# Kernel tuning notes

Measured on AMD Instinct MI355X. Metric: run time of the kernel, lower is better.

The kernel has to match this reference:

```python
import jax, jax.numpy as jnp
import numpy as np

N, E, H, G, L = 50000, 640000, 128, 8, 3

def setup_inputs() -> dict:
    key = jax.random.key(0)
    ks = jax.random.split(key, 10)
    s = 1.0 / np.sqrt(H)
    return {
        "x": jax.random.normal(ks[0], (N, H), jnp.float32),
        "query": jax.random.normal(ks[1], (G, H), jnp.float32),
        "Wl": jax.random.normal(ks[2], (L, H, H), jnp.float32) * s,
        "bl": jax.random.normal(ks[3], (L, H), jnp.float32) * s,
        "Wr": jax.random.normal(ks[4], (L, H, H), jnp.float32) * s,
        "Wlin": jax.random.normal(ks[5], (H, H), jnp.float32) * s,
        "blin": jax.random.normal(ks[6], (H,), jnp.float32) * s,
        "edge_index": jax.random.randint(ks[7], (2, E), 0, N, jnp.int64),
        "batch_vec": jnp.sort(jax.random.randint(ks[8], (N,), 0, G, jnp.int64)),
    }

def reference(x, query, Wl, bl, Wr, Wlin, blin, edge_index, batch_vec):
    src, dst = edge_index[0], edge_index[1]
    n = x.shape[0]
    for i in range(L):
        # SAGEConv(aggr='max'): gather neighbor feats, scatter-max to dst
        m = jax.ops.segment_max(x[src], dst, num_segments=n)  # [N,H]
        m = jnp.where(jnp.isfinite(m), m, 0.0)  # isolated nodes -> 0 (PyG)
        x = jax.nn.relu(m @ Wl[i].T + bl[i] + x @ Wr[i].T)
    x = x @ Wlin.T + blin  # encoder final linear
    # cosine scoring per graph, vectorized via batch_vec
    xn = x / jnp.linalg.norm(x, axis=1, keepdims=True).clip(1e-12)
    qn = query / jnp.linalg.norm(query, axis=1, keepdims=True).clip(1e-12)
    scores = jnp.sum(xn * qn[batch_vec], axis=1)  # [N]
    return scores
```

## Files before the change

kernel.cpp:

```cpp
#include <hip/hip_runtime.h>
#include <math.h>

#define H 128

typedef _Float16 half8 __attribute__((ext_vector_type(8)));
typedef float f32x16 __attribute__((ext_vector_type(16)));

__device__ __forceinline__ half8 h8max(half8 a, half8 b) {
#if defined(__has_builtin) && __has_builtin(__builtin_elementwise_max)
    return __builtin_elementwise_max(a, b);
#else
    half8 r;
#pragma unroll
    for (int j = 0; j < 8; ++j) r[j] = a[j] > b[j] ? a[j] : b[j];
    return r;
#endif
}


__global__ __launch_bounds__(256) void hist_deg(const int* __restrict__ ei, int E,
                                                int* __restrict__ deg) {
    int e = blockIdx.x * 256 + threadIdx.x;
    if (e < E) atomicAdd(&deg[ei[E + e]], 1);
}

__global__ __launch_bounds__(256) void scan_atomic(const int* __restrict__ deg,
                                                   int* __restrict__ offsets,
                                                   int* __restrict__ gcur, int N) {
    __shared__ int buf[256];
    __shared__ int sbase;
    int tid = threadIdx.x;
    int i = blockIdx.x * 256 + tid;
    int v = (i < N) ? deg[i] : 0;
    int incl = v;
    buf[tid] = v;
    __syncthreads();
#pragma unroll
    for (int off = 1; off < 256; off <<= 1) {
        int t = (tid >= off) ? buf[tid - off] : 0;
        __syncthreads();
        incl += t;
        buf[tid] = incl;
        __syncthreads();
    }
    if (tid == 255) sbase = atomicAdd(gcur, incl);
    __syncthreads();
    if (i < N) offsets[i] = sbase + incl - v;
}

__global__ __launch_bounds__(256) void fill_adj(const int* __restrict__ ei, int E,
                                                const int* __restrict__ offsets,
                                                int* __restrict__ cursor,
                                                int* __restrict__ adj) {
    int e = blockIdx.x * 256 + threadIdx.x;
    if (e < E) {
        int s = ei[e];
        int d = ei[E + e];
        int pos = atomicAdd(&cursor[d], 1);
        adj[offsets[d] + pos] = s;
    }
}


__global__ __launch_bounds__(256) void prep_all(
    const float* __restrict__ x, const float* __restrict__ query,
    const float* __restrict__ Wl, const float* __restrict__ Wr,
    const float* __restrict__ Wlin, _Float16* __restrict__ xh,
    _Float16* __restrict__ wimg, float* __restrict__ qn, int n8, int SB, int WB) {
    int b = blockIdx.x;
    int tid = threadIdx.x;
    if (b < SB) {
        int i = b * 256 + tid;
        if (i < n8) {
            const float4* x4 = (const float4*)x;
            float4 u = x4[(size_t)i * 2], v = x4[(size_t)i * 2 + 1];
            float f[8] = {u.x, u.y, u.z, u.w, v.x, v.y, v.z, v.w};
            half8 h;
#pragma unroll
            for (int j = 0; j < 8; ++j) h[j] = (_Float16)f[j];
            *(half8*)(xh + (size_t)i * 8) = h;
        }
    } else if (b < SB + WB) {
        int gidx = (b - SB) * 256 + tid;
        if (gidx < 7 * 2048) {
            int mat = gidx / 2048;
            int rem = gidx - mat * 2048;
            int n = rem >> 4;
            int g = rem & 15;
            const float* src = (mat == 6) ? Wlin
                             : ((mat & 1) ? Wr + (mat >> 1) * H * H
                                          : Wl + (mat >> 1) * H * H);
            const float* p = src + n * H + g * 8;
            half8 h, l;
#pragma unroll
            for (int j = 0; j < 8; ++j) {
                float v = p[j];
                _Float16 hh = (_Float16)v;
                h[j] = hh;
                l[j] = (_Float16)(v - (float)hh);
            }
            int kc4 = g >> 2, gpc = g & 3;
            int posB = (gpc + (n & 3) + ((n >> 2) & 3)) & 3;
            size_t base = (size_t)mat * 32768 + (size_t)kc4 * 8192 + n * 32 + posB * 8;
            *(half8*)(wimg + base) = h;
            *(half8*)(wimg + base + 4096) = l;
        }
    } else {
        int g = b - SB - WB;
        __shared__ float part[4];
        float v = (tid < 128) ? query[g * H + tid] : 0.f;
        float ss = v * v;
#pragma unroll
        for (int off = 32; off > 0; off >>= 1) ss += __shfl_xor(ss, off, 64);
        if ((tid & 63) == 0) part[tid >> 6] = ss;
        __syncthreads();
        float tot = part[0] + part[1];
        if (tid < 128) qn[g * H + tid] = v / fmaxf(sqrtf(tot), 1e-12f);
    }
}


__global__ __launch_bounds__(256) void layer_fused2(
    const half8* __restrict__ Xh, const int* __restrict__ deg,
    const int* __restrict__ offsets, const int* __restrict__ adj,
    const _Float16* __restrict__ Bimg, const float* __restrict__ bias,
    _Float16* __restrict__ Yh, int N) {
    __shared__ __align__(16) _Float16 sU[8192];
    __shared__ __align__(16) _Float16 sB[8192];

    int tid = threadIdx.x;
    int w = tid >> 6;
    int lane = tid & 63;
    int l31 = lane & 31;
    int lhi = lane >> 5;
    int ws = w >> 1;
    int wc = w & 1;
    int n0 = blockIdx.x * 64;

    {
        int lf = tid & 15;
        int grp = tid >> 4;
        const _Float16 ni = (_Float16)(-INFINITY);
        const half8 ninf = {ni, ni, ni, ni, ni, ni, ni, ni};
        const half8 hz = {(_Float16)0.f, (_Float16)0.f, (_Float16)0.f, (_Float16)0.f,
                          (_Float16)0.f, (_Float16)0.f, (_Float16)0.f, (_Float16)0.f};
#pragma unroll
        for (int pp = 0; pp < 2; ++pp) {
            int rowA = grp * 4 + pp * 2;
            int rowB = rowA + 1;
            int nA = n0 + rowA, nB = n0 + rowB;
            int eA = 0, dA = 0, eB = 0, dB = 0;
            if (nA < N) { eA = offsets[nA]; dA = deg[nA]; }
            if (nB < N) { eB = offsets[nB]; dB = deg[nB]; }
            half8 a0 = ninf, a1 = ninf, b0 = ninf, b1 = ninf;
            int itm = dA > dB ? dA : dB;
            for (int base = 0; base < itm; base += 4) {
                bool doA = base < dA, doB = base < dB;
                half8 vA[4], vB[4];
                if (doA) {
#pragma unroll
                    for (int u = 0; u < 4; ++u) {
                        int ee = base + u;
                        int idx = adj[eA + (ee < dA ? ee : dA - 1)];
                        vA[u] = Xh[(size_t)idx * 16 + lf];
                    }
                }
                if (doB) {
#pragma unroll
                    for (int u = 0; u < 4; ++u) {
                        int ee = base + u;
                        int idx = adj[eB + (ee < dB ? ee : dB - 1)];
                        vB[u] = Xh[(size_t)idx * 16 + lf];
                    }
                }
                if (doA) {
                    a0 = h8max(a0, h8max(vA[0], vA[2]));
                    a1 = h8max(a1, h8max(vA[1], vA[3]));
                }
                if (doB) {
                    b0 = h8max(b0, h8max(vB[0], vB[2]));
                    b1 = h8max(b1, h8max(vB[1], vB[3]));
                }
            }
            half8 bestA = (dA > 0) ? h8max(a0, a1) : hz;
            half8 bestB = (dB > 0) ? h8max(b0, b1) : hz;
            *(half8*)&sU[rowA * 128 + (lf ^ (rowA & 15)) * 8] = bestA;
            *(half8*)&sU[rowB * 128 + (lf ^ (rowB & 15)) * 8] = bestB;
        }
    }
    __syncthreads();

    f32x16 acc[2];
#pragma unroll
    for (int nt = 0; nt < 2; ++nt) {
        float bv = bias[wc * 64 + nt * 32 + l31];
#pragma unroll
        for (int r = 0; r < 16; ++r) acc[nt][r] = bv;
    }

    int rl = ws * 32 + l31;

    for (int kc4 = 0; kc4 < 4; ++kc4) {
        if (kc4) __syncthreads();
        {
            const half8* bsrc = (const half8*)(Bimg + (size_t)kc4 * 8192);
            half8* bdst = (half8*)sB;
#pragma unroll
            for (int i = 0; i < 4; ++i) bdst[tid + i * 256] = bsrc[tid + i * 256];
        }
        __syncthreads();
#pragma unroll
        for (int ks = 0; ks < 2; ++ks) {
            int g16 = kc4 * 4 + ks * 2 + lhi;
            int posA = g16 ^ (rl & 15);
            half8 ah = *(const half8*)&sU[rl * 128 + posA * 8];
#pragma unroll
            for (int nt = 0; nt < 2; ++nt) {
                int n = wc * 64 + nt * 32 + l31;
                int gpc = ks * 2 + lhi;
                int posB = (gpc + (n & 3) + ((n >> 2) & 3)) & 3;
                half8 bh = *(const half8*)&sB[n * 32 + posB * 8];
                half8 bl = *(const half8*)&sB[4096 + n * 32 + posB * 8];
                acc[nt] = __builtin_amdgcn_mfma_f32_32x32x16_f16(ah, bh, acc[nt], 0, 0, 0);
                acc[nt] = __builtin_amdgcn_mfma_f32_32x32x16_f16(ah, bl, acc[nt], 0, 0, 0);
            }
        }
    }

    for (int kc4 = 0; kc4 < 4; ++kc4) {
        __syncthreads();
        {
            const half8* bsrc = (const half8*)(Bimg + 32768 + (size_t)kc4 * 8192);
            half8* bdst = (half8*)sB;
#pragma unroll
            for (int i = 0; i < 4; ++i) bdst[tid + i * 256] = bsrc[tid + i * 256];
        }
        if ((kc4 & 1) == 0) {
            int kc64 = kc4 >> 1;
#pragma unroll
            for (int i = 0; i < 2; ++i) {
                int idx = tid + i * 256;
                int row = idx >> 3;
                int gp8 = idx & 7;
                int n = n0 + row;
                half8 h = {(_Float16)0.f, (_Float16)0.f, (_Float16)0.f, (_Float16)0.f,
                           (_Float16)0.f, (_Float16)0.f, (_Float16)0.f, (_Float16)0.f};
                if (n < N) h = Xh[(size_t)n * 16 + kc64 * 8 + gp8];
                int pos8 = (gp8 + (row & 7) + ((row >> 3) & 7)) & 7;
                *(half8*)&sU[row * 72 + pos8 * 8] = h;
            }
        }
        __syncthreads();
#pragma unroll
        for (int ks = 0; ks < 2; ++ks) {
            int gp8 = (kc4 & 1) * 4 + ks * 2 + lhi;
            int posA8 = (gp8 + (rl & 7) + ((rl >> 3) & 7)) & 7;
            half8 ah = *(const half8*)&sU[rl * 72 + posA8 * 8];
#pragma unroll
            for (int nt = 0; nt < 2; ++nt) {
                int n = wc * 64 + nt * 32 + l31;
                int gpc = ks * 2 + lhi;
                int posB = (gpc + (n & 3) + ((n >> 2) & 3)) & 3;
                half8 bh = *(const half8*)&sB[n * 32 + posB * 8];
                half8 bl = *(const half8*)&sB[4096 + n * 32 + posB * 8];
                acc[nt] = __builtin_amdgcn_mfma_f32_32x32x16_f16(ah, bh, acc[nt], 0, 0, 0);
                acc[nt] = __builtin_amdgcn_mfma_f32_32x32x16_f16(ah, bl, acc[nt], 0, 0, 0);
            }
        }
    }

#pragma unroll
    for (int r = 0; r < 16; ++r) {
        int row = n0 + ws * 32 + (r & 3) + 8 * (r >> 2) + 4 * lhi;
        if (row < N) {
#pragma unroll
            for (int nt = 0; nt < 2; ++nt) {
                int col = wc * 64 + nt * 32 + l31;
                Yh[(size_t)row * H + col] = (_Float16)fmaxf(acc[nt][r], 0.f);
            }
        }
    }
}


__global__ __launch_bounds__(256) void final_mfma6(
    const half8* __restrict__ Xh, const _Float16* __restrict__ Bimg,
    const float* __restrict__ blin, const float* __restrict__ qn,
    const int* __restrict__ bv, float* __restrict__ out, int N) {
    __shared__ __align__(16) _Float16 sA[9216];
    __shared__ __align__(16) _Float16 sB[8192];

    int tid = threadIdx.x;
    int w = tid >> 6;
    int lane = tid & 63;
    int l31 = lane & 31;
    int lhi = lane >> 5;
    int n0 = blockIdx.x * 128;

    int arow = n0 + w * 32 + l31;
    arow = arow < N ? arow : N - 1;
    int gl = bv[arow];

    f32x16 acc[4];
#pragma unroll
    for (int nt = 0; nt < 4; ++nt) {
        float b = blin[nt * 32 + l31];
#pragma unroll
        for (int r = 0; r < 16; ++r) acc[nt][r] = b;
    }

    int rl = w * 32 + l31;

    for (int kc4 = 0; kc4 < 4; ++kc4) {
        if (kc4) __syncthreads();
        {
            const half8* bsrc = (const half8*)(Bimg + (size_t)kc4 * 8192);
            half8* bdst = (half8*)sB;
#pragma unroll
            for (int i = 0; i < 4; ++i) bdst[tid + i * 256] = bsrc[tid + i * 256];
        }
        if ((kc4 & 1) == 0) {
            int kc64 = kc4 >> 1;
#pragma unroll
            for (int i = 0; i < 4; ++i) {
                int idx = tid + i * 256;
                int row = idx >> 3;
                int gp8 = idx & 7;
                int n = n0 + row;
                half8 h = {(_Float16)0.f, (_Float16)0.f, (_Float16)0.f, (_Float16)0.f,
                           (_Float16)0.f, (_Float16)0.f, (_Float16)0.f, (_Float16)0.f};
                if (n < N) h = Xh[(size_t)n * 16 + kc64 * 8 + gp8];
                int pos8 = (gp8 + (row & 7) + ((row >> 3) & 7)) & 7;
                *(half8*)&sA[row * 72 + pos8 * 8] = h;
            }
        }
        __syncthreads();
#pragma unroll
        for (int ks = 0; ks < 2; ++ks) {
            int gp8 = (kc4 & 1) * 4 + ks * 2 + lhi;
            int posA8 = (gp8 + (rl & 7) + ((rl >> 3) & 7)) & 7;
            half8 ah = *(const half8*)&sA[rl * 72 + posA8 * 8];
#pragma unroll
            for (int nt = 0; nt < 4; ++nt) {
                int n = nt * 32 + l31;
                int gpc = ks * 2 + lhi;
                int posB = (gpc + (n & 3) + ((n >> 2) & 3)) & 3;
                half8 bh = *(const half8*)&sB[n * 32 + posB * 8];
                half8 bl = *(const half8*)&sB[4096 + n * 32 + posB * 8];
                acc[nt] = __builtin_amdgcn_mfma_f32_32x32x16_f16(ah, bh, acc[nt], 0, 0, 0);
                acc[nt] = __builtin_amdgcn_mfma_f32_32x32x16_f16(ah, bl, acc[nt], 0, 0, 0);
            }
        }
    }

#pragma unroll
    for (int r = 0; r < 16; ++r) {
        int rloc = (r & 3) + 8 * (r >> 2) + 4 * lhi;
        int row = n0 + w * 32 + rloc;
        int g = __shfl(gl, rloc, 32);
        float ss = 0.f, sd = 0.f;
#pragma unroll
        for (int nt = 0; nt < 4; ++nt) {
            float y = acc[nt][r];
            float q = qn[(size_t)g * H + nt * 32 + l31];
            ss = fmaf(y, y, ss);
            sd = fmaf(y, q, sd);
        }
#pragma unroll
        for (int off = 1; off <= 16; off <<= 1) {
            ss += __shfl_xor(ss, off, 64);
            sd += __shfl_xor(sd, off, 64);
        }
        if (l31 == 0 && row < N) out[row] = sd / fmaxf(sqrtf(ss), 1e-12f);
    }
}


extern "C" void kernel_launch(void* const* d_in, const int* in_sizes, int n_in,
                              void* d_out, int out_size, void* d_ws, size_t ws_size,
                              hipStream_t stream) {
    const float* x = (const float*)d_in[0];
    const float* query = (const float*)d_in[1];
    const float* Wl = (const float*)d_in[2];
    const float* bl = (const float*)d_in[3];
    const float* Wr = (const float*)d_in[4];
    const float* Wlin = (const float*)d_in[5];
    const float* blin = (const float*)d_in[6];
    const int* ei = (const int*)d_in[7];
    const int* bv = (const int*)d_in[8];
    float* out = (float*)d_out;

    const int N = in_sizes[0] / H;
    const int E = in_sizes[7] / 2;
    const int G = in_sizes[1] / H;

    char* p = (char*)d_ws;
    auto alloc = [&](size_t bytes) {
        char* r = p;
        p += (bytes + 255) & ~(size_t)255;
        return r;
    };
    int* deg = (int*)alloc((size_t)(2 * N + 1) * sizeof(int));
    int* cursor = deg + N;
    int* gcur = deg + 2 * N;
    int* offsets = (int*)alloc((size_t)N * sizeof(int));
    int* adj = (int*)alloc((size_t)E * sizeof(int));
    float* qn = (float*)alloc((size_t)G * H * sizeof(float));
    _Float16* wimg = (_Float16*)alloc((size_t)7 * 32768 * sizeof(_Float16));
    size_t actH = (size_t)N * H * sizeof(_Float16);
    _Float16* xah = (_Float16*)alloc(actH);
    _Float16* xbh = (_Float16*)alloc(actH);

    hipMemsetAsync(deg, 0, (size_t)(2 * N + 1) * sizeof(int), stream);
    hist_deg<<<(E + 255) / 256, 256, 0, stream>>>(ei, E, deg);
    scan_atomic<<<(N + 255) / 256, 256, 0, stream>>>(deg, offsets, gcur, N);
    fill_adj<<<(E + 255) / 256, 256, 0, stream>>>(ei, E, offsets, cursor, adj);

    const int n8 = N * H / 8;
    const int SB = (n8 + 255) / 256;
    const int WB = (7 * 2048 + 255) / 256;
    prep_all<<<SB + WB + G, 256, 0, stream>>>(x, query, Wl, Wr, Wlin, xah, wimg,
                                              qn, n8, SB, WB);

    const int NGm = (N + 63) / 64;
    const int NGf = (N + 127) / 128;

    layer_fused2<<<NGm, 256, 0, stream>>>(
        (const half8*)xah, deg, offsets, adj, wimg + (size_t)0 * 65536,
        bl + 0 * H, xbh, N);
    layer_fused2<<<NGm, 256, 0, stream>>>(
        (const half8*)xbh, deg, offsets, adj, wimg + (size_t)1 * 65536,
        bl + 1 * H, xah, N);
    layer_fused2<<<NGm, 256, 0, stream>>>(
        (const half8*)xah, deg, offsets, adj, wimg + (size_t)2 * 65536,
        bl + 2 * H, xbh, N);
    final_mfma6<<<NGf, 256, 0, stream>>>(
        (const half8*)xbh, wimg + (size_t)6 * 32768, blin, qn, bv, out, N);
}
```

Measured before the change: 285.1 us.

## Split each node's neighbor max across four lane groups and fold degree histogram into prep

The gather-max stage now processes one destination node at a time per wave. Four 16-lane subgroups each fetch a different neighbor, so each iteration covers 16 edges, and the partial maxima are combined with cross-lane xor shuffles. Previously each group of 16 threads walked two nodes serially, 4 edges at a time. This is meant to raise memory-level parallelism and even out the load across varying degrees, at the cost of serializing 16 nodes per wave and padding work for low-degree nodes. Separately, the degree histogram moves into the prep_all launch to remove one kernel launch.

Result: no change. 280.9 us (-1.5%).

```diff
diff --git a/kernel.cpp b/kernel.cpp
--- a/kernel.cpp
+++ b/kernel.cpp
@@ -5,6 +5,7 @@
 
 typedef _Float16 half8 __attribute__((ext_vector_type(8)));
 typedef float f32x16 __attribute__((ext_vector_type(16)));
+typedef int int4v __attribute__((ext_vector_type(4)));
 
 __device__ __forceinline__ half8 h8max(half8 a, half8 b) {
 #if defined(__has_builtin) && __has_builtin(__builtin_elementwise_max)
@@ -17,12 +18,16 @@
 #endif
 }
 
-
-__global__ __launch_bounds__(256) void hist_deg(const int* __restrict__ ei, int E,
-                                                int* __restrict__ deg) {
-    int e = blockIdx.x * 256 + threadIdx.x;
-    if (e < E) atomicAdd(&deg[ei[E + e]], 1);
-}
+__device__ __forceinline__ half8 h8shfl_xor(half8 v, int mask) {
+    int4v iv;
+    __builtin_memcpy(&iv, &v, 16);
+#pragma unroll
+    for (int j = 0; j < 4; ++j) iv[j] = __shfl_xor(iv[j], mask, 64);
+    half8 r;
+    __builtin_memcpy(&r, &iv, 16);
+    return r;
+}
+
 
 __global__ __launch_bounds__(256) void scan_atomic(const int* __restrict__ deg,
                                                    int* __restrict__ offsets,
@@ -63,14 +68,19 @@
 
 
 __global__ __launch_bounds__(256) void prep_all(
+    const int* __restrict__ ei, int E, int* __restrict__ deg,
     const float* __restrict__ x, const float* __restrict__ query,
     const float* __restrict__ Wl, const float* __restrict__ Wr,
     const float* __restrict__ Wlin, _Float16* __restrict__ xh,
-    _Float16* __restrict__ wimg, float* __restrict__ qn, int n8, int SB, int WB) {
+    _Float16* __restrict__ wimg, float* __restrict__ qn, int n8, int HB, int SB,
+    int WB) {
     int b = blockIdx.x;
     int tid = threadIdx.x;
-    if (b < SB) {
-        int i = b * 256 + tid;
+    if (b < HB) {
+        int e = b * 256 + tid;
+        if (e < E) atomicAdd(&deg[ei[E + e]], 1);
+    } else if (b < HB + SB) {
+        int i = (b - HB) * 256 + tid;
         if (i < n8) {
             const float4* x4 = (const float4*)x;
             float4 u = x4[(size_t)i * 2], v = x4[(size_t)i * 2 + 1];
@@ -80,8 +90,8 @@
             for (int j = 0; j < 8; ++j) h[j] = (_Float16)f[j];
             *(half8*)(xh + (size_t)i * 8) = h;
         }
-    } else if (b < SB + WB) {
-        int gidx = (b - SB) * 256 + tid;
+    } else if (b < HB + SB + WB) {
+        int gidx = (b - HB - SB) * 256 + tid;
         if (gidx < 7 * 2048) {
             int mat = gidx / 2048;
             int rem = gidx - mat * 2048;
@@ -106,7 +116,7 @@
             *(half8*)(wimg + base + 4096) = l;
         }
     } else {
-        int g = b - SB - WB;
+        int g = b - HB - SB - WB;
         __shared__ float part[4];
         float v = (tid < 128) ? query[g * H + tid] : 0.f;
         float ss = v * v;
@@ -120,7 +130,7 @@
 }
 
 
-__global__ __launch_bounds__(256) void layer_fused2(
+__global__ __launch_bounds__(256) void layer_fused3(
     const half8* __restrict__ Xh, const int* __restrict__ deg,
     const int* __restrict__ offsets, const int* __restrict__ adj,
     const _Float16* __restrict__ Bimg, const float* __restrict__ bias,
@@ -138,54 +148,36 @@
     int n0 = blockIdx.x * 64;
 
     {
-        int lf = tid & 15;
-        int grp = tid >> 4;
+        int sub = lane >> 4;
+        int lf = lane & 15;
         const _Float16 ni = (_Float16)(-INFINITY);
         const half8 ninf = {ni, ni, ni, ni, ni, ni, ni, ni};
         const half8 hz = {(_Float16)0.f, (_Float16)0.f, (_Float16)0.f, (_Float16)0.f,
                           (_Float16)0.f, (_Float16)0.f, (_Float16)0.f, (_Float16)0.f};
-#pragma unroll
-        for (int pp = 0; pp < 2; ++pp) {
-            int rowA = grp * 4 + pp * 2;
-            int rowB = rowA + 1;
-            int nA = n0 + rowA, nB = n0 + rowB;
-            int eA = 0, dA = 0, eB = 0, dB = 0;
-            if (nA < N) { eA = offsets[nA]; dA = deg[nA]; }
-            if (nB < N) { eB = offsets[nB]; dB = deg[nB]; }
-            half8 a0 = ninf, a1 = ninf, b0 = ninf, b1 = ninf;
-            int itm = dA > dB ? dA : dB;
-            for (int base = 0; base < itm; base += 4) {
-                bool doA = base < dA, doB = base < dB;
-                half8 vA[4], vB[4];
-                if (doA) {
-#pragma unroll
-                    for (int u = 0; u < 4; ++u) {
-                        int ee = base + u;
-                        int idx = adj[eA + (ee < dA ? ee : dA - 1)];
-                        vA[u] = Xh[(size_t)idx * 16 + lf];
-                    }
+        int nd = n0 + w * 16 + lf;
+        int ndc = nd < N ? nd : N - 1;
+        int e0v = offsets[ndc];
+        int degv = (nd < N) ? deg[ndc] : 0;
+
+        for (int i = 0; i < 16; ++i) {
+            int e0 = __shfl(e0v, i, 64);
+            int d = __shfl(degv, i, 64);
+            int row = w * 16 + i;
+            half8 acc = ninf;
+            for (int base = 0; base < d; base += 16) {
+                half8 v[4];
+#pragma unroll
+                for (int q = 0; q < 4; ++q) {
+                    int j = base + q * 4 + sub;
+                    int idx = adj[e0 + (j < d ? j : d - 1)];
+                    v[q] = Xh[(size_t)idx * 16 + lf];
                 }
-                if (doB) {
-#pragma unroll
-                    for (int u = 0; u < 4; ++u) {
-                        int ee = base + u;
-                        int idx = adj[eB + (ee < dB ? ee : dB - 1)];
-                        vB[u] = Xh[(size_t)idx * 16 + lf];
-                    }
-                }
-                if (doA) {
-                    a0 = h8max(a0, h8max(vA[0], vA[2]));
-                    a1 = h8max(a1, h8max(vA[1], vA[3]));
-                }
-                if (doB) {
-                    b0 = h8max(b0, h8max(vB[0], vB[2]));
-                    b1 = h8max(b1, h8max(vB[1], vB[3]));
-                }
-            }
-            half8 bestA = (dA > 0) ? h8max(a0, a1) : hz;
-            half8 bestB = (dB > 0) ? h8max(b0, b1) : hz;
-            *(half8*)&sU[rowA * 128 + (lf ^ (rowA & 15)) * 8] = bestA;
-            *(half8*)&sU[rowB * 128 + (lf ^ (rowB & 15)) * 8] = bestB;
+                acc = h8max(acc, h8max(h8max(v[0], v[1]), h8max(v[2], v[3])));
+            }
+            acc = h8max(acc, h8shfl_xor(acc, 16));
+            acc = h8max(acc, h8shfl_xor(acc, 32));
+            if (d == 0) acc = hz;
+            if (sub == 0) *(half8*)&sU[row * 128 + (lf ^ (row & 15)) * 8] = acc;
         }
     }
     __syncthreads();
@@ -412,26 +404,27 @@
     _Float16* xbh = (_Float16*)alloc(actH);
 
     hipMemsetAsync(deg, 0, (size_t)(2 * N + 1) * sizeof(int), stream);
-    hist_deg<<<(E + 255) / 256, 256, 0, stream>>>(ei, E, deg);
+
+    const int n8 = N * H / 8;
+    const int HB = (E + 255) / 256;
+    const int SB = (n8 + 255) / 256;
+    const int WB = (7 * 2048 + 255) / 256;
+    prep_all<<<HB + SB + WB + G, 256, 0, stream>>>(ei, E, deg, x, query, Wl, Wr,
+                                                   Wlin, xah, wimg, qn, n8, HB,
+                                                   SB, WB);
     scan_atomic<<<(N + 255) / 256, 256, 0, stream>>>(deg, offsets, gcur, N);
     fill_adj<<<(E + 255) / 256, 256, 0, stream>>>(ei, E, offsets, cursor, adj);
 
-    const int n8 = N * H / 8;
-    const int SB = (n8 + 255) / 256;
-    const int WB = (7 * 2048 + 255) / 256;
-    prep_all<<<SB + WB + G, 256, 0, stream>>>(x, query, Wl, Wr, Wlin, xah, wimg,
-                                              qn, n8, SB, WB);
-
     const int NGm = (N + 63) / 64;
     const int NGf = (N + 127) / 128;
 
-    layer_fused2<<<NGm, 256, 0, stream>>>(
+    layer_fused3<<<NGm, 256, 0, stream>>>(
         (const half8*)xah, deg, offsets, adj, wimg + (size_t)0 * 65536,
         bl + 0 * H, xbh, N);
-    layer_fused2<<<NGm, 256, 0, stream>>>(
+    layer_fused3<<<NGm, 256, 0, stream>>>(
         (const half8*)xbh, deg, offsets, adj, wimg + (size_t)1 * 65536,
         bl + 1 * H, xah, N);
-    layer_fused2<<<NGm, 256, 0, stream>>>(
+    layer_fused3<<<NGm, 256, 0, stream>>>(
         (const half8*)xah, deg, offsets, adj, wimg + (size_t)2 * 65536,
         bl + 2 * H, xbh, N);
     final_mfma6<<<NGf, 256, 0, stream>>>(
```
